# Kernel tuning notes

Hardware: AMD Instinct MI355X
Metric: run time of the kernel (lower is better)

The kernel has to match this reference:

```python
import jax, jax.numpy as jnp
import numpy as np

OUTPUT_SIZE = 50000
HIDDEN = 512


def setup_inputs() -> dict:
    key = jax.random.key(0)
    k1, k2, k3, k4 = jax.random.split(key, 4)
    input_value = jax.random.normal(k1, (4, 2048, HIDDEN), dtype=jnp.float32)
    mask_tensor = jax.random.randint(k2, (4, 2048, 32), 0, OUTPUT_SIZE, dtype=jnp.int64)
    weight = jax.random.normal(k3, (OUTPUT_SIZE, HIDDEN), dtype=jnp.float32)
    bias = jax.random.uniform(k4, (OUTPUT_SIZE,), dtype=jnp.float32)
    return {"input_value": input_value, "mask_tensor": mask_tensor,
            "weight": weight, "bias": bias}


def reference(input_value, mask_tensor, weight, bias):
    # gather per-token candidate weights: [b, s, m, h]
    part_weight = weight[mask_tensor]
    # gather per-token candidate biases: [b, s, m]
    part_bias = bias[mask_tensor]
    out = jnp.einsum('bsh,bsmh->bsm', input_value, part_weight) + part_bias
    return jax.nn.relu(out)
```

## Files before the change

kernel.cpp:

```cpp
#include <hip/hip_runtime.h>
#include <hip/hip_bf16.h>

#define HIDDEN 512
#define M_PER_TOKEN 32
#define BUCKET_CAP 32

typedef _Float16 half8 __attribute__((ext_vector_type(8)));

__global__ __launch_bounds__(256) void prep_kernel(
    const float* __restrict__ input,
    _Float16*    __restrict__ in_h,
    int*         __restrict__ counts,
    int n_chunks, int n_rows)
{
    int i = blockIdx.x * 256 + threadIdx.x;
    if (i < n_chunks) {
        const float4 a = ((const float4*)input)[2 * i];
        const float4 b = ((const float4*)input)[2 * i + 1];
        half8 h;
        h[0] = (_Float16)a.x; h[1] = (_Float16)a.y;
        h[2] = (_Float16)a.z; h[3] = (_Float16)a.w;
        h[4] = (_Float16)b.x; h[5] = (_Float16)b.y;
        h[6] = (_Float16)b.z; h[7] = (_Float16)b.w;
        ((half8*)in_h)[i] = h;
    }
    if (i < n_rows) counts[i] = 0;
}

__global__ __launch_bounds__(256) void scatter_kernel(
    const int* __restrict__ mask,
    int*       __restrict__ counts,
    int*       __restrict__ padded,
    int n_pairs)
{
    int i = blockIdx.x * 256 + threadIdx.x;
    if (i >= n_pairs) return;
    int r = mask[i];
    int slot = atomicAdd(&counts[r], 1);
    if (slot < BUCKET_CAP) padded[(r << 5) + slot] = i;
}

__global__ __launch_bounds__(256) void row_ffn_kernel(
    const _Float16* __restrict__ in_h,
    const float*    __restrict__ weight,
    const float*    __restrict__ bias,
    const int*      __restrict__ counts,
    const int*      __restrict__ padded,
    float*          __restrict__ out,
    int n_rows, int blocks_per_xcd)
{
    const int b    = (int)blockIdx.x;
    const int bsw  = (b & 7) * blocks_per_xcd + (b >> 3);
    const int wave = threadIdx.x >> 6;
    const int lane = threadIdx.x & 63;
    const int s    = lane & 15;
    const int q    = lane >> 4;
    const int r    = bsw * 4 + wave;
    if (r >= n_rows) return;

    int c = counts[r];
    if (c <= 0) return;
    if (c > BUCKET_CAP) c = BUCKET_CAP;

    const float* wbase = weight + (size_t)r * HIDDEN + s * 8;
    float4 w[8];
#pragma unroll
    for (int j = 0; j < 4; ++j) {
        w[2 * j]     = *(const float4*)(wbase + j * 128);
        w[2 * j + 1] = *(const float4*)(wbase + j * 128 + 4);
    }
    const float bv    = bias[r];
    const int*  users = padded + (r << 5);

    for (int u = 0; u < c; u += 4) {
        const int g   = c - u;
        const int off = (q < g) ? q : (g - 1);
        const int pid = users[u + off];

        const _Float16* irow = in_h + (size_t)(pid >> 5) * HIDDEN + s * 8;
        const half8 h0 = *(const half8*)(irow);
        const half8 h1 = *(const half8*)(irow + 128);
        const half8 h2 = *(const half8*)(irow + 256);
        const half8 h3 = *(const half8*)(irow + 384);

        float d0 = (float)h0[0]*w[0].x + (float)h0[1]*w[0].y
                 + (float)h0[2]*w[0].z + (float)h0[3]*w[0].w
                 + (float)h0[4]*w[1].x + (float)h0[5]*w[1].y
                 + (float)h0[6]*w[1].z + (float)h0[7]*w[1].w;
        float d1 = (float)h1[0]*w[2].x + (float)h1[1]*w[2].y
                 + (float)h1[2]*w[2].z + (float)h1[3]*w[2].w
                 + (float)h1[4]*w[3].x + (float)h1[5]*w[3].y
                 + (float)h1[6]*w[3].z + (float)h1[7]*w[3].w;
        float d2 = (float)h2[0]*w[4].x + (float)h2[1]*w[4].y
                 + (float)h2[2]*w[4].z + (float)h2[3]*w[4].w
                 + (float)h2[4]*w[5].x + (float)h2[5]*w[5].y
                 + (float)h2[6]*w[5].z + (float)h2[7]*w[5].w;
        float d3 = (float)h3[0]*w[6].x + (float)h3[1]*w[6].y
                 + (float)h3[2]*w[6].z + (float)h3[3]*w[6].w
                 + (float)h3[4]*w[7].x + (float)h3[5]*w[7].y
                 + (float)h3[6]*w[7].z + (float)h3[7]*w[7].w;
        float d = (d0 + d1) + (d2 + d3);

        d += __shfl_down(d, 8, 16);
        d += __shfl_down(d, 4, 16);
        d += __shfl_down(d, 2, 16);
        d += __shfl_down(d, 1, 16);

        if (s == 0 && q < g) {
            float v = d + bv;
            out[pid] = v > 0.0f ? v : 0.0f;
        }
    }
}

__global__ __launch_bounds__(256) void dynamic_ffn_f32_kernel(
    const float* __restrict__ input,
    const int*   __restrict__ mask,
    const float* __restrict__ weight,
    const float* __restrict__ bias,
    float*       __restrict__ out,
    int n_tokens)
{
    const int token = blockIdx.x;
    if (token >= n_tokens) return;
    const int wave = threadIdx.x >> 6;
    const int lane = threadIdx.x & 63;

    const float* in_row = input + (size_t)token * HIDDEN + lane * 8;
    const float4 x0 = *(const float4*)(in_row);
    const float4 x1 = *(const float4*)(in_row + 4);

    const int* midx = mask + (size_t)token * M_PER_TOKEN + wave * 8;
    float*     orow = out  + (size_t)token * M_PER_TOKEN + wave * 8;

    int idx[8];
#pragma unroll
    for (int j = 0; j < 8; ++j) idx[j] = midx[j];

    float acc[8];
#pragma unroll
    for (int j = 0; j < 8; ++j) {
        const float* w = weight + (size_t)idx[j] * HIDDEN + lane * 8;
        const float4 a = *(const float4*)(w);
        const float4 b = *(const float4*)(w + 4);
        acc[j] = x0.x * a.x + x0.y * a.y + x0.z * a.z + x0.w * a.w
               + x1.x * b.x + x1.y * b.y + x1.z * b.z + x1.w * b.w;
    }
#pragma unroll
    for (int j = 0; j < 8; ++j) {
        float p = acc[j];
#pragma unroll
        for (int off = 32; off > 0; off >>= 1)
            p += __shfl_down(p, off, 64);
        if (lane == 0) {
            float v = p + bias[idx[j]];
            orow[j] = v > 0.0f ? v : 0.0f;
        }
    }
}

extern "C" void kernel_launch(void* const* d_in, const int* in_sizes, int n_in,
                              void* d_out, int out_size, void* d_ws, size_t ws_size,
                              hipStream_t stream) {
    const float* input  = (const float*)d_in[0];
    const int*   mask   = (const int*)  d_in[1];
    const float* weight = (const float*)d_in[2];
    const float* bias   = (const float*)d_in[3];
    float*       out    = (float*)d_out;

    const int n_tokens = in_sizes[0] / HIDDEN;
    const int n_pairs  = in_sizes[1];
    const int n_rows   = in_sizes[2] / HIDDEN;

    const size_t in_h_bytes   = (size_t)in_sizes[0] * sizeof(_Float16);
    const size_t counts_bytes = (size_t)n_rows * sizeof(int);
    const size_t padded_bytes = (size_t)n_rows * BUCKET_CAP * sizeof(int);
    const size_t need = in_h_bytes + counts_bytes + padded_bytes;

    if (ws_size >= need) {
        _Float16* in_h   = (_Float16*)d_ws;
        int*      counts = (int*)((char*)d_ws + in_h_bytes);
        int*      padded = (int*)((char*)d_ws + in_h_bytes + counts_bytes);

        const int n_chunks = in_sizes[0] / 8;
        prep_kernel<<<(n_chunks + 255) / 256, 256, 0, stream>>>(
            input, in_h, counts, n_chunks, n_rows);

        scatter_kernel<<<(n_pairs + 255) / 256, 256, 0, stream>>>(
            mask, counts, padded, n_pairs);

        const int n_wave_rows    = (n_rows + 3) / 4;
        const int blocks_per_xcd = (n_wave_rows + 7) / 8;
        const int grid           = blocks_per_xcd * 8;
        row_ffn_kernel<<<grid, 256, 0, stream>>>(
            in_h, weight, bias, counts, padded, out, n_rows, blocks_per_xcd);
    } else {
        dynamic_ffn_f32_kernel<<<n_tokens, 256, 0, stream>>>(
            input, mask, weight, bias, out, n_tokens);
    }
}
```

Baseline: 204.0 us.

## Speculatively issue first user loads before count and prefetch next user ids

The row kernel now reads the first user id and its input row in parallel with the bucket count, instead of waiting on the count before doing anything. To make that safe, the prep kernel zeroes the first four padded slots of every row. The loop software-pipelines the next group's user-id load. The shuffle reduction is replaced with DPP row operations, and weight rows are loaded nontemporally. Rows with no users now do wasted loads and compute, and rows with fewer than four users rely on the zeroed slots being valid indices.

```diff
diff --git a/kernel.cpp b/kernel.cpp
--- a/kernel.cpp
+++ b/kernel.cpp
@@ -6,11 +6,13 @@
 #define BUCKET_CAP 32
 
 typedef _Float16 half8 __attribute__((ext_vector_type(8)));
+typedef float    f32x4 __attribute__((ext_vector_type(4)));
 
 __global__ __launch_bounds__(256) void prep_kernel(
     const float* __restrict__ input,
     _Float16*    __restrict__ in_h,
     int*         __restrict__ counts,
+    int*         __restrict__ padded,
     int n_chunks, int n_rows)
 {
     int i = blockIdx.x * 256 + threadIdx.x;
@@ -24,7 +26,10 @@
         h[6] = (_Float16)b.z; h[7] = (_Float16)b.w;
         ((half8*)in_h)[i] = h;
     }
-    if (i < n_rows) counts[i] = 0;
+    if (i < n_rows) {
+        counts[i] = 0;
+        *(int4*)(padded + ((size_t)i << 5)) = make_int4(0, 0, 0, 0);
+    }
 }
 
 __global__ __launch_bounds__(256) void scatter_kernel(
@@ -38,6 +43,28 @@
     int r = mask[i];
     int slot = atomicAdd(&counts[r], 1);
     if (slot < BUCKET_CAP) padded[(r << 5) + slot] = i;
+}
+
+template <int CTRL>
+__device__ __forceinline__ float dpp_add(float v) {
+    return v + __int_as_float(__builtin_amdgcn_update_dpp(
+        0, __float_as_int(v), CTRL, 0xF, 0xF, true));
+}
+
+__device__ __forceinline__ float red16(float v) {
+    v = dpp_add<0xB1>(v);
+    v = dpp_add<0x4E>(v);
+    v = dpp_add<0x141>(v);
+    v = dpp_add<0x140>(v);
+    return v;
+}
+
+__device__ __forceinline__ float dot128(const half8 h, const f32x4 wa,
+                                        const f32x4 wb) {
+    return (float)h[0]*wa[0] + (float)h[1]*wa[1]
+         + (float)h[2]*wa[2] + (float)h[3]*wa[3]
+         + (float)h[4]*wb[0] + (float)h[5]*wb[1]
+         + (float)h[6]*wb[2] + (float)h[7]*wb[3];
 }
 
 __global__ __launch_bounds__(256) void row_ffn_kernel(
@@ -58,56 +85,64 @@
     const int r    = bsw * 4 + wave;
     if (r >= n_rows) return;
 
-    int c = counts[r];
-    if (c <= 0) return;
-    if (c > BUCKET_CAP) c = BUCKET_CAP;
+    const int* users = padded + ((size_t)r << 5);
+
+    const int   c_raw = counts[r];
+    const int   pid0  = users[q];
+    const float bv    = bias[r];
 
     const float* wbase = weight + (size_t)r * HIDDEN + s * 8;
-    float4 w[8];
+    f32x4 w[8];
 #pragma unroll
     for (int j = 0; j < 4; ++j) {
-        w[2 * j]     = *(const float4*)(wbase + j * 128);
-        w[2 * j + 1] = *(const float4*)(wbase + j * 128 + 4);
-    }
-    const float bv    = bias[r];
-    const int*  users = padded + (r << 5);
-
-    for (int u = 0; u < c; u += 4) {
+        w[2*j]   = __builtin_nontemporal_load((const f32x4*)(wbase + j*128));
+        w[2*j+1] = __builtin_nontemporal_load((const f32x4*)(wbase + j*128 + 4));
+    }
+
+    const _Float16* irow0 = in_h + (size_t)(pid0 >> 5) * HIDDEN + s * 8;
+    const half8 h0 = *(const half8*)(irow0);
+    const half8 h1 = *(const half8*)(irow0 + 128);
+    const half8 h2 = *(const half8*)(irow0 + 256);
+    const half8 h3 = *(const half8*)(irow0 + 384);
+
+    const int c = (c_raw > BUCKET_CAP) ? BUCKET_CAP : c_raw;
+
+    int pid_n = 0;
+    if (c > 4) {
+        const int g4  = c - 4;
+        const int off = (q < g4) ? q : (g4 - 1);
+        pid_n = users[4 + off];
+    }
+
+    float d = dot128(h0, w[0], w[1]) + dot128(h1, w[2], w[3])
+            + dot128(h2, w[4], w[5]) + dot128(h3, w[6], w[7]);
+    d = red16(d);
+    if (s == 0 && q < c) {
+        float v = d + bv;
+        out[pid0] = v > 0.0f ? v : 0.0f;
+    }
+
+    for (int u = 4; u < c; u += 4) {
         const int g   = c - u;
-        const int off = (q < g) ? q : (g - 1);
-        const int pid = users[u + off];
+        const int pid = pid_n;
 
         const _Float16* irow = in_h + (size_t)(pid >> 5) * HIDDEN + s * 8;
-        const half8 h0 = *(const half8*)(irow);
-        const half8 h1 = *(const half8*)(irow + 128);
-        const half8 h2 = *(const half8*)(irow + 256);
-        const half8 h3 = *(const half8*)(irow + 384);
-
-        float d0 = (float)h0[0]*w[0].x + (float)h0[1]*w[0].y
-                 + (float)h0[2]*w[0].z + (float)h0[3]*w[0].w
-                 + (float)h0[4]*w[1].x + (float)h0[5]*w[1].y
-                 + (float)h0[6]*w[1].z + (float)h0[7]*w[1].w;
-        float d1 = (float)h1[0]*w[2].x + (float)h1[1]*w[2].y
-                 + (float)h1[2]*w[2].z + (float)h1[3]*w[2].w
-                 + (float)h1[4]*w[3].x + (float)h1[5]*w[3].y
-                 + (float)h1[6]*w[3].z + (float)h1[7]*w[3].w;
-        float d2 = (float)h2[0]*w[4].x + (float)h2[1]*w[4].y
-                 + (float)h2[2]*w[4].z + (float)h2[3]*w[4].w
-                 + (float)h2[4]*w[5].x + (float)h2[5]*w[5].y
-                 + (float)h2[6]*w[5].z + (float)h2[7]*w[5].w;
-        float d3 = (float)h3[0]*w[6].x + (float)h3[1]*w[6].y
-                 + (float)h3[2]*w[6].z + (float)h3[3]*w[6].w
-                 + (float)h3[4]*w[7].x + (float)h3[5]*w[7].y
-                 + (float)h3[6]*w[7].z + (float)h3[7]*w[7].w;
-        float d = (d0 + d1) + (d2 + d3);
-
-        d += __shfl_down(d, 8, 16);
-        d += __shfl_down(d, 4, 16);
-        d += __shfl_down(d, 2, 16);
-        d += __shfl_down(d, 1, 16);
-
+        const half8 g0 = *(const half8*)(irow);
+        const half8 g1 = *(const half8*)(irow + 128);
+        const half8 g2 = *(const half8*)(irow + 256);
+        const half8 g3 = *(const half8*)(irow + 384);
+
+        if (u + 4 < c) {
+            const int gn  = c - (u + 4);
+            const int off = (q < gn) ? q : (gn - 1);
+            pid_n = users[u + 4 + off];
+        }
+
+        float e = dot128(g0, w[0], w[1]) + dot128(g1, w[2], w[3])
+                + dot128(g2, w[4], w[5]) + dot128(g3, w[6], w[7]);
+        e = red16(e);
         if (s == 0 && q < g) {
-            float v = d + bv;
+            float v = e + bv;
             out[pid] = v > 0.0f ? v : 0.0f;
         }
     }
@@ -184,7 +219,7 @@
 
         const int n_chunks = in_sizes[0] / 8;
         prep_kernel<<<(n_chunks + 255) / 256, 256, 0, stream>>>(
-            input, in_h, counts, n_chunks, n_rows);
+            input, in_h, counts, padded, n_chunks, n_rows);
 
         scatter_kernel<<<(n_pairs + 255) / 256, 256, 0, stream>>>(
             mask, counts, padded, n_pairs);
```

Result: no change. 202.6 us (-0.7%).
